# Optimization experiments

Measured on AMD Instinct MI355X. Metric: run time of the kernel, lower is better.

## Reference

```python
import jax, jax.numpy as jnp
import numpy as np


def setup_inputs() -> dict:
    key = jax.random.key(0)
    k1, k2, k3, k4, k5 = jax.random.split(key, 5)
    B, Cin, D, H, W = 16, 16, 32, 32, 32
    Cout, Kd = 32, 3
    return {
        "x": jax.random.normal(k1, (B, Cin, D, H, W), dtype=jnp.float32),
        "weight": jax.random.normal(k2, (Cout, Cin, Kd, Kd, Kd), dtype=jnp.float32),
        "conv_bias": jax.random.normal(k3, (Cout,), dtype=jnp.float32),
        "scaling_factor": jax.random.normal(k4, (Cout, 1, 1, 1), dtype=jnp.float32),
        "bias_param": jax.random.normal(k5, (Cout, 1, 1, 1), dtype=jnp.float32),
    }


def reference(x, weight, conv_bias, scaling_factor, bias_param):
    # 3D valid conv, stride 1, NCDHW layout / OIDHW kernel
    y = jax.lax.conv_general_dilated(
        x, weight,
        window_strides=(1, 1, 1),
        padding="VALID",
        dimension_numbers=("NCDHW", "OIDHW", "NCDHW"),
    )
    # per-channel bias, scale, tanh, scale, sigmoid (broadcast over D,H,W)
    y = y + conv_bias[None, :, None, None, None]
    y = jnp.tanh(y * scaling_factor[None]) * bias_param[None]
    return jax.nn.sigmoid(y)
```

## Files before the change

### kernel.cpp

```cpp
#include <hip/hip_runtime.h>

#define NB    16
#define CIN   16
#define COUT  32
#define DIN   32
#define DOUT  30

typedef __attribute__((ext_vector_type(8)))  short  short8;
typedef __attribute__((ext_vector_type(16))) float  f32x16;

static __device__ __forceinline__ unsigned short f2bf_rne(float f) {
    unsigned int u = __builtin_bit_cast(unsigned int, f);
    u += 0x7fffu + ((u >> 16) & 1u);
    return (unsigned short)(u >> 16);
}
static __device__ __forceinline__ float bf2f(unsigned short s) {
    unsigned int u = ((unsigned int)s) << 16;
    return __builtin_bit_cast(float, u);
}

__global__ __launch_bounds__(64) void repack_w(const float* __restrict__ wgt,
                                               short* __restrict__ ws) {
    const int s  = blockIdx.x;
    const int l  = threadIdx.x;
    const int co  = l & 31;
    const int ci0 = (l >> 5) * 8;
    short8 vh, vl;
#pragma unroll
    for (int j = 0; j < 8; ++j) {
        float f = wgt[co * (CIN * 27) + (ci0 + j) * 27 + s];
        unsigned short h = f2bf_rne(f);
        vh[j] = (short)h;
        vl[j] = (short)f2bf_rne(f - bf2f(h));
    }
    ((short8*)ws)[s * 64 + l]            = vh;
    ((short8*)ws)[27 * 64 + s * 64 + l]  = vl;
}

__global__ __launch_bounds__(256) void conv3d_mfma(
    const float* __restrict__ x,
    const short* __restrict__ wsA,
    const float* __restrict__ cbias,
    const float* __restrict__ scal,
    const float* __restrict__ bpar,
    float* __restrict__ out)
{
    __shared__ short sx[2 * 9216];
    __shared__ float sp[96];

    const int htile = blockIdx.x;
    const int d     = blockIdx.y;
    const int b     = blockIdx.z;

    const int tid  = threadIdx.x;
    const int wy   = tid >> 6;
    const int lane = tid & 63;

    if (tid < 32) {
        sp[tid]      = cbias[tid];
        sp[32 + tid] = scal[tid];
        sp[64 + tid] = bpar[tid];
    }

    const int h0 = htile * 4;

    const int xb = b * (CIN * DIN * DIN * DIN);
    for (int c = tid; c < 1152; c += 256) {
        const int hi8 = c & 1;
        const int r2  = c >> 1;
        const int w   = r2 & 31;
        const int rr  = r2 >> 5;
        const int dz  = rr / 6;
        const int row = rr - dz * 6;
        int h_in = h0 + row; if (h_in > 31) h_in = 31;
        const int gbase = xb + (hi8 * 8) * (DIN * DIN * DIN)
                        + (d + dz) * (DIN * DIN) + h_in * DIN + w;
        short8 vh, vl;
#pragma unroll
        for (int j = 0; j < 8; ++j) {
            float f = x[gbase + j * (DIN * DIN * DIN)];
            unsigned short h = f2bf_rne(f);
            vh[j] = (short)h;
            vl[j] = (short)f2bf_rne(f - bf2f(h));
        }
        *(short8*)(sx + c * 8)        = vh;
        *(short8*)(sx + 9216 + c * 8) = vl;
    }
    __syncthreads();

    const int h = h0 + wy;
    if (h >= DOUT) return;

    const int n  = lane & 31;
    const int hi = lane >> 5;

    int wofs[3];
#pragma unroll
    for (int kw = 0; kw < 3; ++kw) {
        int wc = n + kw; if (wc > 31) wc = 31;
        wofs[kw] = wc * 16 + hi * 8;
    }

    f32x16 acc;
#pragma unroll
    for (int i = 0; i < 16; ++i) acc[i] = 0.0f;

    const short8* wa = (const short8*)wsA;
#pragma unroll
    for (int kd = 0; kd < 3; ++kd) {
#pragma unroll
        for (int kh = 0; kh < 3; ++kh) {
            const int rbase = (kd * 6 + wy + kh) * (32 * 16);
#pragma unroll
            for (int kw = 0; kw < 3; ++kw) {
                const int s = kd * 9 + kh * 3 + kw;
                short8 ah = wa[s * 64 + lane];
                short8 al = wa[1728 + s * 64 + lane];
                short8 bh = *(const short8*)(sx + rbase + wofs[kw]);
                short8 bl = *(const short8*)(sx + 9216 + rbase + wofs[kw]);
                acc = __builtin_amdgcn_mfma_f32_32x32x16_bf16(ah, bh, acc, 0, 0, 0);
                acc = __builtin_amdgcn_mfma_f32_32x32x16_bf16(ah, bl, acc, 0, 0, 0);
                acc = __builtin_amdgcn_mfma_f32_32x32x16_bf16(al, bh, acc, 0, 0, 0);
            }
        }
    }

    if (n < DOUT) {
        const int obase = b * (COUT * DOUT * DOUT * DOUT)
                        + d * (DOUT * DOUT) + h * DOUT + n;
#pragma unroll
        for (int r = 0; r < 16; ++r) {
            const int co = (r & 3) + 8 * (r >> 2) + 4 * hi;
            float y  = acc[r] + sp[co];
            float t  = y * sp[32 + co];
            float th = 1.0f - 2.0f / (__expf(2.0f * t) + 1.0f);
            float z  = th * sp[64 + co];
            float rr = 1.0f / (1.0f + __expf(-z));
            out[obase + co * (DOUT * DOUT * DOUT)] = rr;
        }
    }
}

extern "C" void kernel_launch(void* const* d_in, const int* in_sizes, int n_in,
                              void* d_out, int out_size, void* d_ws, size_t ws_size,
                              hipStream_t stream) {
    const float* x     = (const float*)d_in[0];
    const float* wgt   = (const float*)d_in[1];
    const float* cbias = (const float*)d_in[2];
    const float* scal  = (const float*)d_in[3];
    const float* bpar  = (const float*)d_in[4];
    float* out = (float*)d_out;
    short* ws  = (short*)d_ws;

    hipLaunchKernelGGL(repack_w, dim3(27), dim3(64), 0, stream, wgt, ws);
    hipLaunchKernelGGL(conv3d_mfma, dim3(8, DOUT, NB), dim3(256), 0, stream,
                       x, ws, cbias, scal, bpar, out);
}
```

Measured before the change: 144.7 us.

## Pre-split input into bf16 hi/lo workspace and compute two depth slices per block

Adds a prep kernel that converts x once into a global bf16 hi/lo channel-interleaved layout, so the conv kernel only copies ready rows into swizzled LDS instead of redoing strided fp32 loads and splits for every overlapping depth window. Each conv block now computes two output depth slices, reusing each loaded B fragment across both accumulators and halving the grid. This adds a workspace of about 32 MB that must be written and read back, plus fallback paths for smaller workspaces, including a direct fp32 kernel.

```diff
diff --git a/kernel.cpp b/kernel.cpp
--- a/kernel.cpp
+++ b/kernel.cpp
@@ -5,6 +5,7 @@
 #define COUT  32
 #define DIN   32
 #define DOUT  30
+#define XS_OFF 57344
 
 typedef __attribute__((ext_vector_type(8)))  short  short8;
 typedef __attribute__((ext_vector_type(16))) float  f32x16;
@@ -19,39 +20,58 @@
     return __builtin_bit_cast(float, u);
 }
 
-__global__ __launch_bounds__(64) void repack_w(const float* __restrict__ wgt,
-                                               short* __restrict__ ws) {
-    const int s  = blockIdx.x;
-    const int l  = threadIdx.x;
-    const int co  = l & 31;
-    const int ci0 = (l >> 5) * 8;
-    short8 vh, vl;
-#pragma unroll
-    for (int j = 0; j < 8; ++j) {
-        float f = wgt[co * (CIN * 27) + (ci0 + j) * 27 + s];
-        unsigned short h = f2bf_rne(f);
-        vh[j] = (short)h;
-        vl[j] = (short)f2bf_rne(f - bf2f(h));
-    }
-    ((short8*)ws)[s * 64 + l]            = vh;
-    ((short8*)ws)[27 * 64 + s * 64 + l]  = vl;
-}
-
-__global__ __launch_bounds__(256) void conv3d_mfma(
-    const float* __restrict__ x,
-    const short* __restrict__ wsA,
+__global__ __launch_bounds__(256) void prep_kernel(const float* __restrict__ x,
+                                                   const float* __restrict__ wgt,
+                                                   char* __restrict__ ws) {
+    const int bx  = blockIdx.x;
+    const int tid = threadIdx.x;
+    if (bx < 4096) {
+        const int wy = tid >> 6, lane = tid & 63;
+        const int rid = bx * 4 + wy;
+        const int h = rid & 31, d = (rid >> 5) & 31, b = rid >> 10;
+        const int w = lane >> 1, oc = lane & 1;
+        const float* xp = x + ((((size_t)(b * 16 + oc * 8) * 32 + d) * 32 + h) * 32 + w);
+        short8 vh, vl;
+#pragma unroll
+        for (int j = 0; j < 8; ++j) {
+            float f = xp[j * 32768];
+            unsigned short hb = f2bf_rne(f);
+            vh[j] = (short)hb;
+            vl[j] = (short)f2bf_rne(f - bf2f(hb));
+        }
+        char* row = ws + XS_OFF + (size_t)rid * 2048;
+        *(short8*)(row + lane * 16)        = vh;
+        *(short8*)(row + 1024 + lane * 16) = vl;
+    } else if (tid < 64) {
+        const int s = bx - 4096;
+        const int l = tid;
+        const int co = l & 31, ci0 = (l >> 5) * 8;
+        short8 vh, vl;
+#pragma unroll
+        for (int j = 0; j < 8; ++j) {
+            float f = wgt[co * (CIN * 27) + (ci0 + j) * 27 + s];
+            unsigned short hb = f2bf_rne(f);
+            vh[j] = (short)hb;
+            vl[j] = (short)f2bf_rne(f - bf2f(hb));
+        }
+        ((short8*)ws)[s * 64 + l]           = vh;
+        ((short8*)ws)[1728 + s * 64 + l]    = vl;
+    }
+}
+
+__global__ __launch_bounds__(256) void conv_main(
+    const char* __restrict__ ws,
     const float* __restrict__ cbias,
     const float* __restrict__ scal,
     const float* __restrict__ bpar,
     float* __restrict__ out)
 {
-    __shared__ short sx[2 * 9216];
+    __shared__ __align__(16) short sx[24576];
     __shared__ float sp[96];
 
     const int htile = blockIdx.x;
-    const int d     = blockIdx.y;
+    const int d2    = blockIdx.y;
     const int b     = blockIdx.z;
-
     const int tid  = threadIdx.x;
     const int wy   = tid >> 6;
     const int lane = tid & 63;
@@ -62,52 +82,142 @@
         sp[64 + tid] = bpar[tid];
     }
 
+    const int h0 = htile * 4, d0 = d2 * 2;
+    const char* xbase = ws + XS_OFF;
+    const int psw = (lane ^ ((lane >> 3) & 7)) * 8;
+
+#pragma unroll
+    for (int r = wy * 12; r < wy * 12 + 12; ++r) {
+        const int buf = r & 1, pr = r >> 1;
+        const int p = pr / 6, row = pr - p * 6;
+        int hin = h0 + row; if (hin > 31) hin = 31;
+        const int rid = (b * 32 + d0 + p) * 32 + hin;
+        const short8 v = *((const short8*)(xbase + (size_t)rid * 2048 + buf * 1024) + lane);
+        *(short8*)(sx + (pr * 2 + buf) * 512 + psw) = v;
+    }
+    __syncthreads();
+
+    const int h = h0 + wy;
+    if (h >= DOUT) return;
+
+    const int n  = lane & 31;
+    const int oc = lane >> 5;
+    int cofs[3];
+#pragma unroll
+    for (int kw = 0; kw < 3; ++kw) {
+        int wc = n + kw; if (wc > 31) wc = 31;
+        const int c = 2 * wc + oc;
+        cofs[kw] = (c ^ ((c >> 3) & 7)) * 8;
+    }
+
+    f32x16 acc0, acc1;
+#pragma unroll
+    for (int i = 0; i < 16; ++i) { acc0[i] = 0.0f; acc1[i] = 0.0f; }
+
+    const short8* wa = (const short8*)ws;
+#pragma unroll
+    for (int kh = 0; kh < 3; ++kh) {
+        const int rowi = wy + kh;
+#pragma unroll
+        for (int kw = 0; kw < 3; ++kw) {
+            short8 bh[4], bl[4];
+#pragma unroll
+            for (int p = 0; p < 4; ++p) {
+                const short* slot = sx + ((p * 6 + rowi) * 2) * 512;
+                bh[p] = *(const short8*)(slot + cofs[kw]);
+                bl[p] = *(const short8*)(slot + 512 + cofs[kw]);
+            }
+#pragma unroll
+            for (int kd = 0; kd < 3; ++kd) {
+                const int s = kd * 9 + kh * 3 + kw;
+                short8 ah = wa[s * 64 + lane];
+                short8 al = wa[1728 + s * 64 + lane];
+                acc0 = __builtin_amdgcn_mfma_f32_32x32x16_bf16(ah, bh[kd],     acc0, 0, 0, 0);
+                acc1 = __builtin_amdgcn_mfma_f32_32x32x16_bf16(ah, bh[kd + 1], acc1, 0, 0, 0);
+                acc0 = __builtin_amdgcn_mfma_f32_32x32x16_bf16(ah, bl[kd],     acc0, 0, 0, 0);
+                acc1 = __builtin_amdgcn_mfma_f32_32x32x16_bf16(ah, bl[kd + 1], acc1, 0, 0, 0);
+                acc0 = __builtin_amdgcn_mfma_f32_32x32x16_bf16(al, bh[kd],     acc0, 0, 0, 0);
+                acc1 = __builtin_amdgcn_mfma_f32_32x32x16_bf16(al, bh[kd + 1], acc1, 0, 0, 0);
+            }
+        }
+    }
+
+    if (n < DOUT) {
+        const int ob = b * (COUT * 27000) + h * 30 + n;
+#pragma unroll
+        for (int r = 0; r < 16; ++r) {
+            const int co = (r & 3) + 8 * (r >> 2) + 4 * oc;
+            float y0 = acc0[r] + sp[co];
+            float t0 = y0 * sp[32 + co];
+            float th0 = 1.0f - 2.0f / (__expf(2.0f * t0) + 1.0f);
+            float z0 = th0 * sp[64 + co];
+            out[ob + co * 27000 + d0 * 900] = 1.0f / (1.0f + __expf(-z0));
+
+            float y1 = acc1[r] + sp[co];
+            float t1 = y1 * sp[32 + co];
+            float th1 = 1.0f - 2.0f / (__expf(2.0f * t1) + 1.0f);
+            float z1 = th1 * sp[64 + co];
+            out[ob + co * 27000 + (d0 + 1) * 900] = 1.0f / (1.0f + __expf(-z1));
+        }
+    }
+}
+
+__global__ __launch_bounds__(64) void repack_w_fb(const float* __restrict__ wgt,
+                                                  short* __restrict__ ws) {
+    const int s = blockIdx.x, l = threadIdx.x;
+    const int co = l & 31, ci0 = (l >> 5) * 8;
+    short8 vh, vl;
+#pragma unroll
+    for (int j = 0; j < 8; ++j) {
+        float f = wgt[co * (CIN * 27) + (ci0 + j) * 27 + s];
+        unsigned short hb = f2bf_rne(f);
+        vh[j] = (short)hb;
+        vl[j] = (short)f2bf_rne(f - bf2f(hb));
+    }
+    ((short8*)ws)[s * 64 + l]           = vh;
+    ((short8*)ws)[27 * 64 + s * 64 + l] = vl;
+}
+
+__global__ __launch_bounds__(256) void conv3d_mfma_fb(
+    const float* __restrict__ x, const short* __restrict__ wsA,
+    const float* __restrict__ cbias, const float* __restrict__ scal,
+    const float* __restrict__ bpar, float* __restrict__ out)
+{
+    __shared__ short sx[2 * 9216];
+    __shared__ float sp[96];
+    const int htile = blockIdx.x, d = blockIdx.y, b = blockIdx.z;
+    const int tid = threadIdx.x, wy = tid >> 6, lane = tid & 63;
+    if (tid < 32) { sp[tid] = cbias[tid]; sp[32 + tid] = scal[tid]; sp[64 + tid] = bpar[tid]; }
     const int h0 = htile * 4;
-
     const int xb = b * (CIN * DIN * DIN * DIN);
     for (int c = tid; c < 1152; c += 256) {
-        const int hi8 = c & 1;
-        const int r2  = c >> 1;
-        const int w   = r2 & 31;
-        const int rr  = r2 >> 5;
-        const int dz  = rr / 6;
-        const int row = rr - dz * 6;
+        const int hi8 = c & 1, r2 = c >> 1, w = r2 & 31, rr = r2 >> 5;
+        const int dz = rr / 6, row = rr - dz * 6;
         int h_in = h0 + row; if (h_in > 31) h_in = 31;
-        const int gbase = xb + (hi8 * 8) * (DIN * DIN * DIN)
-                        + (d + dz) * (DIN * DIN) + h_in * DIN + w;
+        const int gbase = xb + (hi8 * 8) * (DIN * DIN * DIN) + (d + dz) * (DIN * DIN) + h_in * DIN + w;
         short8 vh, vl;
 #pragma unroll
         for (int j = 0; j < 8; ++j) {
             float f = x[gbase + j * (DIN * DIN * DIN)];
-            unsigned short h = f2bf_rne(f);
-            vh[j] = (short)h;
-            vl[j] = (short)f2bf_rne(f - bf2f(h));
-        }
-        *(short8*)(sx + c * 8)        = vh;
+            unsigned short hb = f2bf_rne(f);
+            vh[j] = (short)hb; vl[j] = (short)f2bf_rne(f - bf2f(hb));
+        }
+        *(short8*)(sx + c * 8) = vh;
         *(short8*)(sx + 9216 + c * 8) = vl;
     }
     __syncthreads();
-
     const int h = h0 + wy;
     if (h >= DOUT) return;
-
-    const int n  = lane & 31;
-    const int hi = lane >> 5;
-
+    const int n = lane & 31, hi = lane >> 5;
     int wofs[3];
 #pragma unroll
-    for (int kw = 0; kw < 3; ++kw) {
-        int wc = n + kw; if (wc > 31) wc = 31;
-        wofs[kw] = wc * 16 + hi * 8;
-    }
-
+    for (int kw = 0; kw < 3; ++kw) { int wc = n + kw; if (wc > 31) wc = 31; wofs[kw] = wc * 16 + hi * 8; }
     f32x16 acc;
 #pragma unroll
     for (int i = 0; i < 16; ++i) acc[i] = 0.0f;
-
     const short8* wa = (const short8*)wsA;
 #pragma unroll
-    for (int kd = 0; kd < 3; ++kd) {
+    for (int kd = 0; kd < 3; ++kd)
 #pragma unroll
         for (int kh = 0; kh < 3; ++kh) {
             const int rbase = (kd * 6 + wy + kh) * (32 * 16);
@@ -123,20 +233,69 @@
                 acc = __builtin_amdgcn_mfma_f32_32x32x16_bf16(al, bh, acc, 0, 0, 0);
             }
         }
-    }
-
     if (n < DOUT) {
-        const int obase = b * (COUT * DOUT * DOUT * DOUT)
-                        + d * (DOUT * DOUT) + h * DOUT + n;
+        const int obase = b * (COUT * 27000) + d * 900 + h * 30 + n;
 #pragma unroll
         for (int r = 0; r < 16; ++r) {
             const int co = (r & 3) + 8 * (r >> 2) + 4 * hi;
-            float y  = acc[r] + sp[co];
-            float t  = y * sp[32 + co];
+            float y = acc[r] + sp[co];
+            float t = y * sp[32 + co];
             float th = 1.0f - 2.0f / (__expf(2.0f * t) + 1.0f);
-            float z  = th * sp[64 + co];
-            float rr = 1.0f / (1.0f + __expf(-z));
-            out[obase + co * (DOUT * DOUT * DOUT)] = rr;
+            float z = th * sp[64 + co];
+            out[obase + co * 27000] = 1.0f / (1.0f + __expf(-z));
+        }
+    }
+}
+
+__global__ __launch_bounds__(256) void conv3d_direct_fb(
+    const float* __restrict__ x, const float* __restrict__ wgt,
+    const float* __restrict__ cbias, const float* __restrict__ scal,
+    const float* __restrict__ bpar, float* __restrict__ out)
+{
+    __shared__ float sw[CIN * 27];
+    const int bx = blockIdx.x, co = blockIdx.y, b = blockIdx.z;
+    const int tid = threadIdx.y * 32 + threadIdx.x;
+    for (int i = tid; i < CIN * 27; i += 256) sw[i] = wgt[co * (CIN * 27) + i];
+    __syncthreads();
+    const float bias = cbias[co], s = scal[co], bp = bpar[co];
+    const int dt = bx & 7, ht = bx >> 3;
+    const int d0 = dt * 4, h = ht * 8 + threadIdx.y, w = threadIdx.x;
+    if (w >= DOUT || h >= DOUT) return;
+    int rowoff[6];
+#pragma unroll
+    for (int dz = 0; dz < 6; ++dz) { int dd = d0 + dz; if (dd > 31) dd = 31; rowoff[dz] = dd * 1024; }
+    float acc[4] = {0.f, 0.f, 0.f, 0.f};
+    const int xb = b * (CIN * 32768);
+    for (int ci = 0; ci < CIN; ++ci) {
+        const int cioff = xb + ci * 32768;
+        const float* swc = &sw[ci * 27];
+#pragma unroll
+        for (int kh = 0; kh < 3; ++kh) {
+            const int hbase = cioff + (h + kh) * DIN + w;
+#pragma unroll
+            for (int kw = 0; kw < 3; ++kw) {
+                float xv[6];
+#pragma unroll
+                for (int dz = 0; dz < 6; ++dz) xv[dz] = x[hbase + kw + rowoff[dz]];
+#pragma unroll
+                for (int kd = 0; kd < 3; ++kd) {
+                    const float wv = swc[(kd * 3 + kh) * 3 + kw];
+#pragma unroll
+                    for (int dd = 0; dd < 4; ++dd) acc[dd] = fmaf(xv[dd + kd], wv, acc[dd]);
+                }
+            }
+        }
+    }
+    const int obase = (b * COUT + co) * 27000 + h * 30 + w;
+#pragma unroll
+    for (int dd = 0; dd < 4; ++dd) {
+        const int d = d0 + dd;
+        if (d < DOUT) {
+            float y = acc[dd] + bias;
+            float t = y * s;
+            float th = 1.0f - 2.0f / (__expf(2.0f * t) + 1.0f);
+            float z = th * bp;
+            out[obase + d * 900] = 1.0f / (1.0f + __expf(-z));
         }
     }
 }
@@ -150,9 +309,20 @@
     const float* scal  = (const float*)d_in[3];
     const float* bpar  = (const float*)d_in[4];
     float* out = (float*)d_out;
-    short* ws  = (short*)d_ws;
-
-    hipLaunchKernelGGL(repack_w, dim3(27), dim3(64), 0, stream, wgt, ws);
-    hipLaunchKernelGGL(conv3d_mfma, dim3(8, DOUT, NB), dim3(256), 0, stream,
-                       x, ws, cbias, scal, bpar, out);
-}
+
+    const size_t need_full = (size_t)XS_OFF + (size_t)16384 * 2048;
+    if (ws_size >= need_full) {
+        char* ws = (char*)d_ws;
+        hipLaunchKernelGGL(prep_kernel, dim3(4096 + 27), dim3(256), 0, stream, x, wgt, ws);
+        hipLaunchKernelGGL(conv_main, dim3(8, 15, NB), dim3(256), 0, stream,
+                           ws, cbias, scal, bpar, out);
+    } else if (ws_size >= 55296) {
+        short* ws = (short*)d_ws;
+        hipLaunchKernelGGL(repack_w_fb, dim3(27), dim3(64), 0, stream, wgt, ws);
+        hipLaunchKernelGGL(conv3d_mfma_fb, dim3(8, DOUT, NB), dim3(256), 0, stream,
+                           x, ws, cbias, scal, bpar, out);
+    } else {
+        hipLaunchKernelGGL(conv3d_direct_fb, dim3(32, COUT, NB), dim3(32, 8), 0, stream,
+                           x, wgt, cbias, scal, bpar, out);
+    }
+}
```

After: 146.8 us. About the same (+1.4%).

## Stage weights in LDS, load input to registers, compute two depth slices per block

Applied to the files above, without the earlier changes.

Drops the separate weight-repack kernel. Each block now converts the weights to split bf16 hi/lo form and stores them in shared memory. Input rows are read straight from global memory into registers, and the kw shifts are done with ds_bpermute lane rotations instead of an LDS input tile. Each block computes two output depth slices with two accumulators, so each loaded input plane serves two kd taps and the weight LDS reads are shared across both. The cost is redundant weight conversion in every block (54KB of LDS), more registers, and strided global reads of the input.

```diff
diff --git a/kernel.cpp b/kernel.cpp
--- a/kernel.cpp
+++ b/kernel.cpp
@@ -1,12 +1,13 @@
 #include <hip/hip_runtime.h>
 
-#define NB    16
 #define CIN   16
 #define COUT  32
 #define DIN   32
 #define DOUT  30
+#define NB    16
 
 typedef __attribute__((ext_vector_type(8)))  short  short8;
+typedef __attribute__((ext_vector_type(4)))  int    int4v;
 typedef __attribute__((ext_vector_type(16))) float  f32x16;
 
 static __device__ __forceinline__ unsigned short f2bf_rne(float f) {
@@ -18,39 +19,29 @@
     unsigned int u = ((unsigned int)s) << 16;
     return __builtin_bit_cast(float, u);
 }
-
-__global__ __launch_bounds__(64) void repack_w(const float* __restrict__ wgt,
-                                               short* __restrict__ ws) {
-    const int s  = blockIdx.x;
-    const int l  = threadIdx.x;
-    const int co  = l & 31;
-    const int ci0 = (l >> 5) * 8;
-    short8 vh, vl;
+static __device__ __forceinline__ short8 lane_pull(short8 v, int bidx) {
+    int4v a = __builtin_bit_cast(int4v, v);
 #pragma unroll
-    for (int j = 0; j < 8; ++j) {
-        float f = wgt[co * (CIN * 27) + (ci0 + j) * 27 + s];
-        unsigned short h = f2bf_rne(f);
-        vh[j] = (short)h;
-        vl[j] = (short)f2bf_rne(f - bf2f(h));
-    }
-    ((short8*)ws)[s * 64 + l]            = vh;
-    ((short8*)ws)[27 * 64 + s * 64 + l]  = vl;
+    for (int t = 0; t < 4; ++t)
+        a[t] = __builtin_amdgcn_ds_bpermute(bidx, a[t]);
+    return __builtin_bit_cast(short8, a);
 }
 
-__global__ __launch_bounds__(256) void conv3d_mfma(
+__global__ __launch_bounds__(256) void conv_wlds(
     const float* __restrict__ x,
-    const short* __restrict__ wsA,
+    const float* __restrict__ wgt,
     const float* __restrict__ cbias,
     const float* __restrict__ scal,
     const float* __restrict__ bpar,
     float* __restrict__ out)
 {
-    __shared__ short sx[2 * 9216];
+    __shared__ __align__(16) short swh[13824];
+    __shared__ __align__(16) short swl[13824];
     __shared__ float sp[96];
 
-    const int htile = blockIdx.x;
-    const int d     = blockIdx.y;
-    const int b     = blockIdx.z;
+    const int ht = blockIdx.x;
+    const int d2 = blockIdx.y;
+    const int b  = blockIdx.z;
 
     const int tid  = threadIdx.x;
     const int wy   = tid >> 6;
@@ -62,81 +53,95 @@
         sp[64 + tid] = bpar[tid];
     }
 
-    const int h0 = htile * 4;
-
-    const int xb = b * (CIN * DIN * DIN * DIN);
-    for (int c = tid; c < 1152; c += 256) {
-        const int hi8 = c & 1;
-        const int r2  = c >> 1;
-        const int w   = r2 & 31;
-        const int rr  = r2 >> 5;
-        const int dz  = rr / 6;
-        const int row = rr - dz * 6;
-        int h_in = h0 + row; if (h_in > 31) h_in = 31;
-        const int gbase = xb + (hi8 * 8) * (DIN * DIN * DIN)
-                        + (d + dz) * (DIN * DIN) + h_in * DIN + w;
+    for (int e = tid; e < 1728; e += 256) {
+        const int s = e >> 6, l = e & 63;
+        const int co = l & 31, ci0 = (l >> 5) * 8;
         short8 vh, vl;
 #pragma unroll
         for (int j = 0; j < 8; ++j) {
-            float f = x[gbase + j * (DIN * DIN * DIN)];
-            unsigned short h = f2bf_rne(f);
-            vh[j] = (short)h;
-            vl[j] = (short)f2bf_rne(f - bf2f(h));
+            float f = wgt[co * (CIN * 27) + (ci0 + j) * 27 + s];
+            unsigned short hb = f2bf_rne(f);
+            vh[j] = (short)hb;
+            vl[j] = (short)f2bf_rne(f - bf2f(hb));
         }
-        *(short8*)(sx + c * 8)        = vh;
-        *(short8*)(sx + 9216 + c * 8) = vl;
+        *(short8*)(swh + e * 8) = vh;
+        *(short8*)(swl + e * 8) = vl;
     }
     __syncthreads();
 
-    const int h = h0 + wy;
+    const int h0 = ht * 4, d0 = d2 * 2;
+    const int h  = h0 + wy;
     if (h >= DOUT) return;
 
     const int n  = lane & 31;
-    const int hi = lane >> 5;
+    const int oc = lane >> 5;
+    const int bidx = ((n < 31) ? (lane + 1) : lane) * 4;
 
-    int wofs[3];
+    const float* xb = x + (size_t)b * (CIN * 32768) + oc * 8 * 32768 + d0 * 1024 + n;
+
+    f32x16 acc0, acc1;
 #pragma unroll
-    for (int kw = 0; kw < 3; ++kw) {
-        int wc = n + kw; if (wc > 31) wc = 31;
-        wofs[kw] = wc * 16 + hi * 8;
-    }
+    for (int i = 0; i < 16; ++i) { acc0[i] = 0.0f; acc1[i] = 0.0f; }
 
-    f32x16 acc;
 #pragma unroll
-    for (int i = 0; i < 16; ++i) acc[i] = 0.0f;
-
-    const short8* wa = (const short8*)wsA;
+    for (int kh = 0; kh < 3; ++kh) {
+        const float* xr = xb + (h + kh) * 32;
+        short8 fh[4], fl[4];
 #pragma unroll
-    for (int kd = 0; kd < 3; ++kd) {
+        for (int q = 0; q < 4; ++q) {
+            const float* xp = xr + q * 1024;
+            float v[8];
 #pragma unroll
-        for (int kh = 0; kh < 3; ++kh) {
-            const int rbase = (kd * 6 + wy + kh) * (32 * 16);
+            for (int j = 0; j < 8; ++j) v[j] = xp[j * 32768];
+            short8 vh, vl;
 #pragma unroll
-            for (int kw = 0; kw < 3; ++kw) {
+            for (int j = 0; j < 8; ++j) {
+                unsigned short hb = f2bf_rne(v[j]);
+                vh[j] = (short)hb;
+                vl[j] = (short)f2bf_rne(v[j] - bf2f(hb));
+            }
+            fh[q] = vh; fl[q] = vl;
+        }
+#pragma unroll
+        for (int kw = 0; kw < 3; ++kw) {
+            if (kw > 0) {
+#pragma unroll
+                for (int q = 0; q < 4; ++q) {
+                    fh[q] = lane_pull(fh[q], bidx);
+                    fl[q] = lane_pull(fl[q], bidx);
+                }
+            }
+#pragma unroll
+            for (int kd = 0; kd < 3; ++kd) {
                 const int s = kd * 9 + kh * 3 + kw;
-                short8 ah = wa[s * 64 + lane];
-                short8 al = wa[1728 + s * 64 + lane];
-                short8 bh = *(const short8*)(sx + rbase + wofs[kw]);
-                short8 bl = *(const short8*)(sx + 9216 + rbase + wofs[kw]);
-                acc = __builtin_amdgcn_mfma_f32_32x32x16_bf16(ah, bh, acc, 0, 0, 0);
-                acc = __builtin_amdgcn_mfma_f32_32x32x16_bf16(ah, bl, acc, 0, 0, 0);
-                acc = __builtin_amdgcn_mfma_f32_32x32x16_bf16(al, bh, acc, 0, 0, 0);
+                short8 ah = *(const short8*)(swh + (s * 64 + lane) * 8);
+                short8 al = *(const short8*)(swl + (s * 64 + lane) * 8);
+                acc0 = __builtin_amdgcn_mfma_f32_32x32x16_bf16(ah, fh[kd],     acc0, 0, 0, 0);
+                acc1 = __builtin_amdgcn_mfma_f32_32x32x16_bf16(ah, fh[kd + 1], acc1, 0, 0, 0);
+                acc0 = __builtin_amdgcn_mfma_f32_32x32x16_bf16(ah, fl[kd],     acc0, 0, 0, 0);
+                acc1 = __builtin_amdgcn_mfma_f32_32x32x16_bf16(ah, fl[kd + 1], acc1, 0, 0, 0);
+                acc0 = __builtin_amdgcn_mfma_f32_32x32x16_bf16(al, fh[kd],     acc0, 0, 0, 0);
+                acc1 = __builtin_amdgcn_mfma_f32_32x32x16_bf16(al, fh[kd + 1], acc1, 0, 0, 0);
             }
         }
     }
 
     if (n < DOUT) {
-        const int obase = b * (COUT * DOUT * DOUT * DOUT)
-                        + d * (DOUT * DOUT) + h * DOUT + n;
+        const int ob = b * (COUT * 27000) + h * 30 + n;
 #pragma unroll
         for (int r = 0; r < 16; ++r) {
-            const int co = (r & 3) + 8 * (r >> 2) + 4 * hi;
-            float y  = acc[r] + sp[co];
-            float t  = y * sp[32 + co];
-            float th = 1.0f - 2.0f / (__expf(2.0f * t) + 1.0f);
-            float z  = th * sp[64 + co];
-            float rr = 1.0f / (1.0f + __expf(-z));
-            out[obase + co * (DOUT * DOUT * DOUT)] = rr;
+            const int co = (r & 3) + 8 * (r >> 2) + 4 * oc;
+            float y0 = acc0[r] + sp[co];
+            float t0 = y0 * sp[32 + co];
+            float th0 = 1.0f - 2.0f / (__expf(2.0f * t0) + 1.0f);
+            float z0 = th0 * sp[64 + co];
+            out[ob + co * 27000 + d0 * 900] = 1.0f / (1.0f + __expf(-z0));
+
+            float y1 = acc1[r] + sp[co];
+            float t1 = y1 * sp[32 + co];
+            float th1 = 1.0f - 2.0f / (__expf(2.0f * t1) + 1.0f);
+            float z1 = th1 * sp[64 + co];
+            out[ob + co * 27000 + (d0 + 1) * 900] = 1.0f / (1.0f + __expf(-z1));
         }
     }
 }
@@ -150,9 +155,7 @@
     const float* scal  = (const float*)d_in[3];
     const float* bpar  = (const float*)d_in[4];
     float* out = (float*)d_out;
-    short* ws  = (short*)d_ws;
 
-    hipLaunchKernelGGL(repack_w, dim3(27), dim3(64), 0, stream, wgt, ws);
-    hipLaunchKernelGGL(conv3d_mfma, dim3(8, DOUT, NB), dim3(256), 0, stream,
-                       x, ws, cbias, scal, bpar, out);
+    hipLaunchKernelGGL(conv_wlds, dim3(8, 15, NB), dim3(256), 0, stream,
+                       x, wgt, cbias, scal, bpar, out);
 }
```

After: 194.0 us. 1.34x slower.
